# Kernel tuning notes

Hardware: AMD Instinct MI355X
Metric: run time of the kernel (lower is better)

Reference implementation:

```python
import jax, jax.numpy as jnp
import numpy as np

H = 16          # n_heads
D_MODEL = 1024
DK = D_MODEL // H  # 64
N = 2048        # total tokens (module flattens batch*seq)
NEG = -1000000000.0


def setup_inputs() -> dict:
    key = jax.random.key(0)
    ks = jax.random.split(key, 12)
    s = 1.0 / np.sqrt(D_MODEL)
    inp = {
        "query": jax.random.normal(ks[0], (N, D_MODEL), jnp.float32),
        "key": jax.random.normal(ks[1], (N, D_MODEL), jnp.float32),
        "value": jax.random.normal(ks[2], (N, D_MODEL), jnp.float32),
        "mask": jax.random.randint(ks[3], (1, N), 0, 2, jnp.int32),
        "Wq": jax.random.normal(ks[4], (D_MODEL, D_MODEL), jnp.float32) * s,
        "bq": jax.random.normal(ks[5], (D_MODEL,), jnp.float32) * 0.01,
        "Wk": jax.random.normal(ks[6], (D_MODEL, D_MODEL), jnp.float32) * s,
        "bk": jax.random.normal(ks[7], (D_MODEL,), jnp.float32) * 0.01,
        "Wv": jax.random.normal(ks[8], (D_MODEL, D_MODEL), jnp.float32) * s,
        "bv": jax.random.normal(ks[9], (D_MODEL,), jnp.float32) * 0.01,
        "Wo": jax.random.normal(ks[10], (D_MODEL, D_MODEL), jnp.float32) * s,
        "bo": jax.random.normal(ks[11], (D_MODEL,), jnp.float32) * 0.01,
    }
    return inp


def reference(query, key, value, mask, Wq, bq, Wk, bk, Wv, bv, Wo, bo):
    # Linear projections (torch Linear: x @ W.T + b), then split heads: (N, d_model) -> (h, N, d_k)
    def split_heads(x):
        return x.reshape(-1, H, DK).transpose(1, 0, 2)

    q = split_heads(query @ Wq.T + bq)
    k = split_heads(key @ Wk.T + bk)
    v = split_heads(value @ Wv.T + bv)

    # scaled dot-product attention: scores (h, N, N)
    scores = jnp.einsum("hnd,hmd->hnm", q, k) / jnp.sqrt(jnp.asarray(DK, q.dtype))
    # mask: (1, N) --unsqueeze(1)--> (1, 1, N), broadcast over (h, N, N)
    scores = jnp.where(mask[None, :, :] == 0, jnp.asarray(NEG, scores.dtype), scores)
    p_attn = jax.nn.softmax(scores, axis=-1)  # dropout identity (eval mode)

    x = jnp.einsum("hnm,hmd->hnd", p_attn, v)  # (h, N, d_k)
    x = x.transpose(1, 0, 2).reshape(-1, H * DK)  # (N, d_model)
    out = x @ Wo.T + bo
    return (out, p_attn)
```

## Files before the change

kernel.cpp:

```cpp
#include <hip/hip_runtime.h>


#define NTOK 2048
#define DMODEL 1024
#define NHEAD 16
#define DKH 64

typedef __attribute__((ext_vector_type(8))) short bf16x8;
typedef __attribute__((ext_vector_type(4))) float f32x4;

#define WAITVMC(n)                                          \
  do {                                                      \
    asm volatile("s_waitcnt vmcnt(" n ")" ::: "memory");    \
    __builtin_amdgcn_sched_barrier(0);                      \
  } while (0)
#define BARRIER()                                           \
  do {                                                      \
    __builtin_amdgcn_s_barrier();                           \
    __builtin_amdgcn_sched_barrier(0);                      \
  } while (0)

__device__ __forceinline__ unsigned short f2bf(float x) {
  unsigned int u = __builtin_bit_cast(unsigned int, x);
  u += 0x7fffu + ((u >> 16) & 1u);
  return (unsigned short)(u >> 16);
}

__device__ __forceinline__ void gl16(const void* g, void* l) {
  __builtin_amdgcn_global_load_lds((const __attribute__((address_space(1))) void*)g,
                                   (__attribute__((address_space(3))) void*)l, 16, 0, 0);
}

template<int ROWS>
__device__ __forceinline__ void stage_async(const unsigned short* src, int ld,
                                            char* lds, int w, int lane) {
  constexpr int RPW = ROWS / 4;
#pragma unroll
  for (int i = 0; i < RPW / 8; ++i) {
    const int row = w * RPW + i * 8 + (lane >> 3);
    const unsigned short* g = src + (size_t)row * ld + (((lane & 7) ^ (row & 7)) * 8);
    gl16(g, lds + (size_t)(w * RPW + i * 8) * 128);
  }
}

__device__ __forceinline__ bf16x8 ldsfrag(const char* lds, int r, int kb) {
  return *(const bf16x8*)(lds + r * 128 + (kb ^ ((r & 7) << 4)));
}

struct CvtP {
  const float* src[7];
  unsigned short* dst[7];
  int n8[8];
  const int* mask;
  float* mbias;
};
__global__ __launch_bounds__(256) void cvt_all(CvtP P) {
  const int a = blockIdx.z;
  const int i = blockIdx.x * 256 + threadIdx.x;
  if (i >= P.n8[a]) return;
  if (a == 7) {
#pragma unroll
    for (int r = 0; r < 8; ++r) {
      int j = i * 8 + r;
      P.mbias[j] = P.mask[j] ? 0.0f : -1e30f;
    }
    return;
  }
  const float4* s = (const float4*)P.src[a];
  float4 v0 = s[i * 2], v1 = s[i * 2 + 1];
  ushort4 h0, h1;
  h0.x = f2bf(v0.x); h0.y = f2bf(v0.y); h0.z = f2bf(v0.z); h0.w = f2bf(v0.w);
  h1.x = f2bf(v1.x); h1.y = f2bf(v1.y); h1.z = f2bf(v1.z); h1.w = f2bf(v1.w);
  ((ushort4*)P.dst[a])[i * 2] = h0;
  ((ushort4*)P.dst[a])[i * 2 + 1] = h1;
}

struct GemmP2 {
  const unsigned short* A[3];
  const unsigned short* B[3];
  const float* bias[3];
  unsigned short* Cb16;
  float* Cf32;
  unsigned short* VTd;
  long long sC;
  int lda, ldb, ldc, Nn, K;
};

template<int BM, bool OUTF32, bool VTRANS>
__global__ __launch_bounds__(256) void gemm_glds(GemmP2 P) {
  constexpr int BN = 128, WN = 64, FN = 4;
  constexpr int WM = BM / 2, FM = WM / 16;
  __shared__ char ldsA[BM * 128];
  __shared__ char ldsB[BN * 128];
  const int tid = threadIdx.x;
  const int lane = tid & 63, w = tid >> 6;
  const int l15 = lane & 15, lhi = lane >> 4;
  const int z = blockIdx.z;
  const int zi = (gridDim.z == 3) ? z : 0;
  const int ntn = P.Nn / BN;
  const int m0 = ((int)blockIdx.x / ntn) * BM;
  const int n0 = ((int)blockIdx.x % ntn) * BN;
  const unsigned short* Ab = P.A[zi] + (size_t)m0 * P.lda;
  const unsigned short* Bb = P.B[zi] + (size_t)n0 * P.ldb;
  const int wm = w >> 1, wn = w & 1;

  f32x4 acc[FM][FN] = {};
  for (int k0 = 0; k0 < P.K; k0 += 64) {
    stage_async<BM>(Ab + k0, P.lda, ldsA, w, lane);
    stage_async<BN>(Bb + k0, P.ldb, ldsB, w, lane);
    __syncthreads();
#pragma unroll
    for (int kk = 0; kk < 2; ++kk) {
      const int kb = kk * 64 + lhi * 16;
      bf16x8 a[FM], b[FN];
#pragma unroll
      for (int i = 0; i < FM; ++i) a[i] = ldsfrag(ldsA, wm * WM + i * 16 + l15, kb);
#pragma unroll
      for (int j = 0; j < FN; ++j) b[j] = ldsfrag(ldsB, wn * WN + j * 16 + l15, kb);
#pragma unroll
      for (int i = 0; i < FM; ++i)
#pragma unroll
        for (int j = 0; j < FN; ++j)
          acc[i][j] = __builtin_amdgcn_mfma_f32_16x16x32_bf16(a[i], b[j], acc[i][j], 0, 0, 0);
    }
    __syncthreads();
  }

  const int rbase = m0 + wm * WM + lhi * 4;
  const int cbase = n0 + wn * WN + l15;
  if (VTRANS && z == 2) {
#pragma unroll
    for (int j = 0; j < FN; ++j) {
      const int col = cbase + j * 16;
      const float badd = P.bias[zi][col];
#pragma unroll
      for (int i = 0; i < FM; ++i) {
        ushort4 t;
        t.x = f2bf(acc[i][j][0] + badd); t.y = f2bf(acc[i][j][1] + badd);
        t.z = f2bf(acc[i][j][2] + badd); t.w = f2bf(acc[i][j][3] + badd);
        *(ushort4*)(P.VTd + (size_t)col * NTOK + rbase + i * 16) = t;
      }
    }
    return;
  }
#pragma unroll
  for (int j = 0; j < FN; ++j) {
    const int col = cbase + j * 16;
    const float badd = P.bias[zi] ? P.bias[zi][col] : 0.0f;
#pragma unroll
    for (int i = 0; i < FM; ++i) {
#pragma unroll
      for (int rg = 0; rg < 4; ++rg) {
        const int row = rbase + i * 16 + rg;
        const float v = acc[i][j][rg] + badd;
        if constexpr (OUTF32)
          P.Cf32[(size_t)row * P.ldc + col] = v;
        else
          P.Cb16[(size_t)z * P.sC + (size_t)row * P.ldc + col] = f2bf(v);
      }
    }
  }
}

__global__ __launch_bounds__(512, 4) void attn7(const unsigned short* __restrict__ QP,
                                                const unsigned short* __restrict__ KP,
                                                const unsigned short* __restrict__ VT,
                                                const float* __restrict__ mbias,
                                                float* __restrict__ p,
                                                unsigned short* __restrict__ XB) {
  __shared__ char ldsK[2][2][64 * 128];
  __shared__ char ldsV[2][2][64 * 128];
  __shared__ char ldsP[2][64 * 128];
  const int tid = threadIdx.x;
  const int lane = tid & 63, w = tid >> 6;
  const int wm = w & 3, jg = w >> 2;
  const int l15 = lane & 15, lhi = lane >> 4;
  const int id = blockIdx.x;
  const int h = 2 * (id & 7) + ((id >> 3) & 1);
  const int q0 = (id >> 4) * 64;
  const int mrow = wm * 16 + l15;
  constexpr float CEXP = 0.1803368801111204f;

  {
    const int row = w * 8 + (lane >> 3);
    const unsigned short* g =
        QP + (size_t)(q0 + row) * DMODEL + h * DKH + (((lane & 7) ^ (row & 7)) * 8);
    gl16(g, ldsP[0] + (size_t)(w * 8) * 128);
  }
  __syncthreads();
  bf16x8 qf0 = ldsfrag(ldsP[0], mrow, lhi * 16);
  bf16x8 qf1 = ldsfrag(ldsP[0], mrow, 64 + lhi * 16);

  const unsigned short* Kh = KP + (size_t)(jg * 1024) * DMODEL + h * DKH;
  const unsigned short* Vh = VT + (size_t)h * DKH * NTOK + jg * 1024;
  const float* mbh = mbias + jg * 1024;

  float rsum = 0.0f;
  stage_async<64>(Kh, DMODEL, ldsK[jg][0], wm, lane);
  float4 m4n[4];
#pragma unroll
  for (int js = 0; js < 4; ++js) m4n[js] = *(const float4*)(mbh + js * 16 + lhi * 4);
  int b = 0;
  for (int it = 0; it < 16; ++it) {
    WAITVMC("0");
    BARRIER();
    if (it < 15)
      stage_async<64>(Kh + (size_t)(it + 1) * 64 * DMODEL, DMODEL, ldsK[jg][b ^ 1], wm, lane);
    float4 m4c[4];
#pragma unroll
    for (int js = 0; js < 4; ++js) m4c[js] = m4n[js];
    if (it < 15) {
      const float* mb = mbh + (it + 1) * 64;
#pragma unroll
      for (int js = 0; js < 4; ++js) m4n[js] = *(const float4*)(mb + js * 16 + lhi * 4);
    }
    __builtin_amdgcn_sched_barrier(0);
    f32x4 sacc[4] = {};
#pragma unroll
    for (int kk = 0; kk < 2; ++kk)
#pragma unroll
      for (int js = 0; js < 4; ++js) {
        bf16x8 kf = ldsfrag(ldsK[jg][b], js * 16 + l15, kk * 64 + lhi * 16);
        sacc[js] = __builtin_amdgcn_mfma_f32_16x16x32_bf16(kf, kk ? qf1 : qf0, sacc[js], 0, 0, 0);
      }
#pragma unroll
    for (int js = 0; js < 4; ++js) {
      rsum += exp2f(sacc[js][0] * CEXP + m4c[js].x);
      rsum += exp2f(sacc[js][1] * CEXP + m4c[js].y);
      rsum += exp2f(sacc[js][2] * CEXP + m4c[js].z);
      rsum += exp2f(sacc[js][3] * CEXP + m4c[js].w);
    }
    b ^= 1;
  }
  rsum += __shfl_xor(rsum, 16, 64);
  rsum += __shfl_xor(rsum, 32, 64);

  float* ldsR = (float*)ldsP[0];
  BARRIER();
  if (lane < 16) ldsR[jg * 64 + mrow] = rsum;
  BARRIER();
  const float rtot = ldsR[mrow] + ldsR[64 + mrow];
  const float lr = -log2f(rtot);

  f32x4 xacc[4] = {};
  stage_async<64>(Kh, DMODEL, ldsK[jg][0], wm, lane);
  stage_async<64>(Vh, NTOK, ldsV[jg][0], wm, lane);
#pragma unroll
  for (int js = 0; js < 4; ++js) m4n[js] = *(const float4*)(mbh + js * 16 + lhi * 4);
  b = 0;
  for (int it = 0; it < 16; ++it) {
    const int j0 = it * 64;
    if (it == 0) { WAITVMC("0"); } else { WAITVMC("4"); }
    BARRIER();
    if (it < 15) {
      stage_async<64>(Kh + (size_t)(j0 + 64) * DMODEL, DMODEL, ldsK[jg][b ^ 1], wm, lane);
      stage_async<64>(Vh + j0 + 64, NTOK, ldsV[jg][b ^ 1], wm, lane);
    }
    float4 m4c[4];
#pragma unroll
    for (int js = 0; js < 4; ++js) m4c[js] = m4n[js];
    if (it < 15) {
      const float* mb = mbh + (it + 1) * 64;
#pragma unroll
      for (int js = 0; js < 4; ++js) m4n[js] = *(const float4*)(mb + js * 16 + lhi * 4);
    }
    __builtin_amdgcn_sched_barrier(0);
    f32x4 sacc[4] = {};
#pragma unroll
    for (int kk = 0; kk < 2; ++kk)
#pragma unroll
      for (int js = 0; js < 4; ++js) {
        bf16x8 kf = ldsfrag(ldsK[jg][b], js * 16 + l15, kk * 64 + lhi * 16);
        sacc[js] = __builtin_amdgcn_mfma_f32_16x16x32_bf16(kf, kk ? qf1 : qf0, sacc[js], 0, 0, 0);
      }
#pragma unroll
    for (int js = 0; js < 4; ++js) {
      f32x4 e;
      e[0] = exp2f(sacc[js][0] * CEXP + (m4c[js].x + lr));
      e[1] = exp2f(sacc[js][1] * CEXP + (m4c[js].y + lr));
      e[2] = exp2f(sacc[js][2] * CEXP + (m4c[js].z + lr));
      e[3] = exp2f(sacc[js][3] * CEXP + (m4c[js].w + lr));
      ushort4 pb;
      pb.x = f2bf(e[0]); pb.y = f2bf(e[1]); pb.z = f2bf(e[2]); pb.w = f2bf(e[3]);
      *(ushort4*)(ldsP[jg] + mrow * 128 + ((js * 32 + lhi * 8) ^ ((mrow & 7) << 4))) = pb;
    }
#pragma unroll
    for (int jk = 0; jk < 2; ++jk) {
      bf16x8 pf = ldsfrag(ldsP[jg], mrow, jk * 64 + lhi * 16);
#pragma unroll
      for (int dd = 0; dd < 4; ++dd) {
        bf16x8 vf = ldsfrag(ldsV[jg][b], dd * 16 + l15, jk * 64 + lhi * 16);
        xacc[dd] = __builtin_amdgcn_mfma_f32_16x16x32_bf16(vf, pf, xacc[dd], 0, 0, 0);
      }
    }
#pragma unroll
    for (int r = 0; r < 4; ++r) {
      const int row = wm * 16 + r * 4 + lhi;
      const uint2 u =
          *(const uint2*)(ldsP[jg] + row * 128 + ((l15 * 8) ^ ((row & 7) << 4)));
      f32x4 f;
      f[0] = __builtin_bit_cast(float, u.x << 16);
      f[1] = __builtin_bit_cast(float, u.x & 0xffff0000u);
      f[2] = __builtin_bit_cast(float, u.y << 16);
      f[3] = __builtin_bit_cast(float, u.y & 0xffff0000u);
      __builtin_nontemporal_store(
          f, (f32x4*)(p + ((size_t)h * NTOK + q0 + row) * NTOK + jg * 1024 + j0 + l15 * 4));
    }
    b ^= 1;
  }

  float* ldsX = (float*)ldsK;
  BARRIER();
  if (jg == 1) {
#pragma unroll
    for (int dd = 0; dd < 4; ++dd) {
      const int off = (mrow * 256 + ((dd * 64 + lhi * 16) ^ ((mrow & 7) << 4))) >> 2;
      *(f32x4*)(ldsX + off) = xacc[dd];
    }
  }
  BARRIER();
  if (jg == 0) {
    unsigned short* xrow = XB + (size_t)(q0 + mrow) * DMODEL + h * DKH;
#pragma unroll
    for (int dd = 0; dd < 4; ++dd) {
      const int off = (mrow * 256 + ((dd * 64 + lhi * 16) ^ ((mrow & 7) << 4))) >> 2;
      f32x4 o = xacc[dd] + *(const f32x4*)(ldsX + off);
      ushort4 xb;
      xb.x = f2bf(o[0]); xb.y = f2bf(o[1]); xb.z = f2bf(o[2]); xb.w = f2bf(o[3]);
      *(ushort4*)(xrow + dd * 16 + lhi * 4) = xb;
    }
  }
}

extern "C" void kernel_launch(void* const* d_in, const int* in_sizes, int n_in,
                              void* d_out, int out_size, void* d_ws, size_t ws_size,
                              hipStream_t stream) {
  (void)in_sizes; (void)n_in; (void)out_size; (void)ws_size;
  const float* query = (const float*)d_in[0];
  const float* key_  = (const float*)d_in[1];
  const float* value = (const float*)d_in[2];
  const int*   mask  = (const int*)d_in[3];
  const float* Wq = (const float*)d_in[4];
  const float* bq = (const float*)d_in[5];
  const float* Wk = (const float*)d_in[6];
  const float* bk = (const float*)d_in[7];
  const float* Wv = (const float*)d_in[8];
  const float* bv = (const float*)d_in[9];
  const float* Wo = (const float*)d_in[10];
  const float* bo = (const float*)d_in[11];

  float* out = (float*)d_out;
  float* p = out + (size_t)NTOK * DMODEL;

  char* ws = (char*)d_ws;
  unsigned short* QP  = (unsigned short*)(ws);
  unsigned short* KP  = (unsigned short*)(ws + (4u << 20));
  unsigned short* VT  = (unsigned short*)(ws + (8u << 20));
  unsigned short* XB  = (unsigned short*)(ws + (12u << 20));
  unsigned short* qB  = (unsigned short*)(ws + (16u << 20));
  unsigned short* kB  = (unsigned short*)(ws + (20u << 20));
  unsigned short* vB  = (unsigned short*)(ws + (24u << 20));
  unsigned short* WqB = (unsigned short*)(ws + (28u << 20));
  unsigned short* WkB = (unsigned short*)(ws + (30u << 20));
  unsigned short* WvB = (unsigned short*)(ws + (32u << 20));
  unsigned short* WoB = (unsigned short*)(ws + (34u << 20));
  float* mbias = (float*)(ws + (36u << 20));

  {
    CvtP C = {};
    C.src[0] = query; C.dst[0] = qB;  C.n8[0] = NTOK * DMODEL / 8;
    C.src[1] = key_;  C.dst[1] = kB;  C.n8[1] = NTOK * DMODEL / 8;
    C.src[2] = value; C.dst[2] = vB;  C.n8[2] = NTOK * DMODEL / 8;
    C.src[3] = Wq;    C.dst[3] = WqB; C.n8[3] = DMODEL * DMODEL / 8;
    C.src[4] = Wk;    C.dst[4] = WkB; C.n8[4] = DMODEL * DMODEL / 8;
    C.src[5] = Wv;    C.dst[5] = WvB; C.n8[5] = DMODEL * DMODEL / 8;
    C.src[6] = Wo;    C.dst[6] = WoB; C.n8[6] = DMODEL * DMODEL / 8;
    C.n8[7] = NTOK / 8;
    C.mask = mask; C.mbias = mbias;
    cvt_all<<<dim3(1024, 1, 8), 256, 0, stream>>>(C);
  }
  {
    GemmP2 P = {};
    P.A[0] = qB; P.A[1] = kB; P.A[2] = vB;
    P.B[0] = WqB; P.B[1] = WkB; P.B[2] = WvB;
    P.bias[0] = bq; P.bias[1] = bk; P.bias[2] = bv;
    P.Cb16 = QP; P.VTd = VT; P.sC = (long long)NTOK * DMODEL;
    P.lda = DMODEL; P.ldb = DMODEL; P.ldc = DMODEL; P.Nn = DMODEL; P.K = DMODEL;
    gemm_glds<128, false, true>
        <<<dim3((NTOK / 128) * (DMODEL / 128), 1, 3), 256, 0, stream>>>(P);
  }
  attn7<<<dim3(512), 512, 0, stream>>>(QP, KP, VT, mbias, p, XB);
  {
    GemmP2 P = {};
    P.A[0] = XB; P.B[0] = WoB; P.bias[0] = bo;
    P.Cf32 = out; P.sC = 0;
    P.lda = DMODEL; P.ldb = DMODEL; P.ldc = DMODEL; P.Nn = DMODEL; P.K = DMODEL;
    gemm_glds<64, true, false>
        <<<dim3((NTOK / 64) * (DMODEL / 128), 1, 1), 256, 0, stream>>>(P);
  }
}
```

Measured before the change: 148.2 us.

## Rewrite attention kernel with 32x32x16 MFMA tiles and 4-wave blocks

```diff
diff --git a/kernel.cpp b/kernel.cpp
--- a/kernel.cpp
+++ b/kernel.cpp
@@ -8,6 +8,7 @@
 
 typedef __attribute__((ext_vector_type(8))) short bf16x8;
 typedef __attribute__((ext_vector_type(4))) float f32x4;
+typedef __attribute__((ext_vector_type(16))) float f32x16;
 
 #define WAITVMC(n)                                          \
   do {                                                      \
@@ -25,16 +26,19 @@
   u += 0x7fffu + ((u >> 16) & 1u);
   return (unsigned short)(u >> 16);
 }
+__device__ __forceinline__ unsigned int pkbf(float a, float b) {
+  return (unsigned int)f2bf(a) | ((unsigned int)f2bf(b) << 16);
+}
 
 __device__ __forceinline__ void gl16(const void* g, void* l) {
   __builtin_amdgcn_global_load_lds((const __attribute__((address_space(1))) void*)g,
                                    (__attribute__((address_space(3))) void*)l, 16, 0, 0);
 }
 
-template<int ROWS>
+template<int ROWS, int NW>
 __device__ __forceinline__ void stage_async(const unsigned short* src, int ld,
                                             char* lds, int w, int lane) {
-  constexpr int RPW = ROWS / 4;
+  constexpr int RPW = ROWS / NW;
 #pragma unroll
   for (int i = 0; i < RPW / 8; ++i) {
     const int row = w * RPW + i * 8 + (lane >> 3);
@@ -106,8 +110,8 @@
 
   f32x4 acc[FM][FN] = {};
   for (int k0 = 0; k0 < P.K; k0 += 64) {
-    stage_async<BM>(Ab + k0, P.lda, ldsA, w, lane);
-    stage_async<BN>(Bb + k0, P.ldb, ldsB, w, lane);
+    stage_async<BM, 4>(Ab + k0, P.lda, ldsA, w, lane);
+    stage_async<BN, 4>(Bb + k0, P.ldb, ldsB, w, lane);
     __syncthreads();
 #pragma unroll
     for (int kk = 0; kk < 2; ++kk) {
@@ -162,172 +166,185 @@
   }
 }
 
-__global__ __launch_bounds__(512, 4) void attn7(const unsigned short* __restrict__ QP,
+__global__ __launch_bounds__(256, 2) void attn8(const unsigned short* __restrict__ QP,
                                                 const unsigned short* __restrict__ KP,
                                                 const unsigned short* __restrict__ VT,
                                                 const float* __restrict__ mbias,
                                                 float* __restrict__ p,
                                                 unsigned short* __restrict__ XB) {
-  __shared__ char ldsK[2][2][64 * 128];
-  __shared__ char ldsV[2][2][64 * 128];
-  __shared__ char ldsP[2][64 * 128];
+  __shared__ char LDS[81920];
   const int tid = threadIdx.x;
   const int lane = tid & 63, w = tid >> 6;
-  const int wm = w & 3, jg = w >> 2;
-  const int l15 = lane & 15, lhi = lane >> 4;
+  const int rg = w >> 1, jg = w & 1;
+  const int m31 = lane & 31, hi = lane >> 5;
   const int id = blockIdx.x;
   const int h = 2 * (id & 7) + ((id >> 3) & 1);
   const int q0 = (id >> 4) * 64;
-  const int mrow = wm * 16 + l15;
+  const int row_q = rg * 32 + m31;
+  const int swq = (row_q & 7) << 4;
+  const int swm = (m31 & 7) << 4;
   constexpr float CEXP = 0.1803368801111204f;
 
-  {
-    const int row = w * 8 + (lane >> 3);
-    const unsigned short* g =
-        QP + (size_t)(q0 + row) * DMODEL + h * DKH + (((lane & 7) ^ (row & 7)) * 8);
-    gl16(g, ldsP[0] + (size_t)(w * 8) * 128);
-  }
+  char* ldsKb[2] = {LDS + jg * 16384, LDS + jg * 16384 + 8192};
+  char* ldsVb[2] = {LDS + 32768 + jg * 16384, LDS + 32768 + jg * 16384 + 8192};
+  char* ldsPj = LDS + 65536 + jg * 8192;
+  char* ldsQ = LDS + 65536;
+  float* ldsR = (float*)(LDS + 65536 + 8192);
+
+  stage_async<64, 4>(QP + (size_t)q0 * DMODEL + h * DKH, DMODEL, ldsQ, w, lane);
   __syncthreads();
-  bf16x8 qf0 = ldsfrag(ldsP[0], mrow, lhi * 16);
-  bf16x8 qf1 = ldsfrag(ldsP[0], mrow, 64 + lhi * 16);
+  bf16x8 qf[4];
+#pragma unroll
+  for (int kt = 0; kt < 4; ++kt)
+    qf[kt] = *(const bf16x8*)(ldsQ + row_q * 128 + ((kt * 32 + hi * 16) ^ swq));
 
   const unsigned short* Kh = KP + (size_t)(jg * 1024) * DMODEL + h * DKH;
   const unsigned short* Vh = VT + (size_t)h * DKH * NTOK + jg * 1024;
   const float* mbh = mbias + jg * 1024;
 
   float rsum = 0.0f;
-  stage_async<64>(Kh, DMODEL, ldsK[jg][0], wm, lane);
-  float4 m4n[4];
-#pragma unroll
-  for (int js = 0; js < 4; ++js) m4n[js] = *(const float4*)(mbh + js * 16 + lhi * 4);
+  float4 m4[8];
+  stage_async<64, 2>(Kh, DMODEL, ldsKb[0], rg, lane);
+#pragma unroll
+  for (int q = 0; q < 8; ++q)
+    m4[q] = *(const float4*)(mbh + (q >> 2) * 32 + (q & 3) * 8 + hi * 4);
   int b = 0;
   for (int it = 0; it < 16; ++it) {
-    WAITVMC("0");
+    WAITVMC("8");
     BARRIER();
     if (it < 15)
-      stage_async<64>(Kh + (size_t)(it + 1) * 64 * DMODEL, DMODEL, ldsK[jg][b ^ 1], wm, lane);
-    float4 m4c[4];
-#pragma unroll
-    for (int js = 0; js < 4; ++js) m4c[js] = m4n[js];
+      stage_async<64, 2>(Kh + (size_t)(it + 1) * 64 * DMODEL, DMODEL, ldsKb[b ^ 1], rg, lane);
+    __builtin_amdgcn_sched_barrier(0);
+    f32x16 s0 = {}, s1 = {};
+#pragma unroll
+    for (int kt = 0; kt < 4; ++kt) {
+      bf16x8 k0 = *(const bf16x8*)(ldsKb[b] + m31 * 128 + ((kt * 32 + hi * 16) ^ swm));
+      bf16x8 k1 = *(const bf16x8*)(ldsKb[b] + (32 + m31) * 128 + ((kt * 32 + hi * 16) ^ swm));
+      s0 = __builtin_amdgcn_mfma_f32_32x32x16_bf16(k0, qf[kt], s0, 0, 0, 0);
+      s1 = __builtin_amdgcn_mfma_f32_32x32x16_bf16(k1, qf[kt], s1, 0, 0, 0);
+    }
+#pragma unroll
+    for (int rq = 0; rq < 4; ++rq) {
+      rsum += exp2f(s0[rq * 4 + 0] * CEXP + m4[rq].x) + exp2f(s0[rq * 4 + 1] * CEXP + m4[rq].y) +
+              exp2f(s0[rq * 4 + 2] * CEXP + m4[rq].z) + exp2f(s0[rq * 4 + 3] * CEXP + m4[rq].w);
+      rsum += exp2f(s1[rq * 4 + 0] * CEXP + m4[4 + rq].x) + exp2f(s1[rq * 4 + 1] * CEXP + m4[4 + rq].y) +
+              exp2f(s1[rq * 4 + 2] * CEXP + m4[4 + rq].z) + exp2f(s1[rq * 4 + 3] * CEXP + m4[4 + rq].w);
+    }
     if (it < 15) {
-      const float* mb = mbh + (it + 1) * 64;
-#pragma unroll
-      for (int js = 0; js < 4; ++js) m4n[js] = *(const float4*)(mb + js * 16 + lhi * 4);
-    }
-    __builtin_amdgcn_sched_barrier(0);
-    f32x4 sacc[4] = {};
-#pragma unroll
-    for (int kk = 0; kk < 2; ++kk)
-#pragma unroll
-      for (int js = 0; js < 4; ++js) {
-        bf16x8 kf = ldsfrag(ldsK[jg][b], js * 16 + l15, kk * 64 + lhi * 16);
-        sacc[js] = __builtin_amdgcn_mfma_f32_16x16x32_bf16(kf, kk ? qf1 : qf0, sacc[js], 0, 0, 0);
-      }
-#pragma unroll
-    for (int js = 0; js < 4; ++js) {
-      rsum += exp2f(sacc[js][0] * CEXP + m4c[js].x);
-      rsum += exp2f(sacc[js][1] * CEXP + m4c[js].y);
-      rsum += exp2f(sacc[js][2] * CEXP + m4c[js].z);
-      rsum += exp2f(sacc[js][3] * CEXP + m4c[js].w);
+      const float* mb2 = mbh + (it + 1) * 64;
+#pragma unroll
+      for (int q = 0; q < 8; ++q)
+        m4[q] = *(const float4*)(mb2 + (q >> 2) * 32 + (q & 3) * 8 + hi * 4);
     }
     b ^= 1;
   }
-  rsum += __shfl_xor(rsum, 16, 64);
   rsum += __shfl_xor(rsum, 32, 64);
-
-  float* ldsR = (float*)ldsP[0];
+  if (lane < 32) ldsR[jg * 64 + row_q] = rsum;
   BARRIER();
-  if (lane < 16) ldsR[jg * 64 + mrow] = rsum;
-  BARRIER();
-  const float rtot = ldsR[mrow] + ldsR[64 + mrow];
-  const float lr = -log2f(rtot);
-
-  f32x4 xacc[4] = {};
-  stage_async<64>(Kh, DMODEL, ldsK[jg][0], wm, lane);
-  stage_async<64>(Vh, NTOK, ldsV[jg][0], wm, lane);
-#pragma unroll
-  for (int js = 0; js < 4; ++js) m4n[js] = *(const float4*)(mbh + js * 16 + lhi * 4);
+  const float lr = -log2f(ldsR[row_q] + ldsR[64 + row_q]);
+
+  f32x16 x0 = {}, x1 = {};
+  stage_async<64, 2>(Kh, DMODEL, ldsKb[0], rg, lane);
+  stage_async<64, 2>(Vh, NTOK, ldsVb[0], rg, lane);
+#pragma unroll
+  for (int q = 0; q < 8; ++q)
+    m4[q] = *(const float4*)(mbh + (q >> 2) * 32 + (q & 3) * 8 + hi * 4);
   b = 0;
   for (int it = 0; it < 16; ++it) {
     const int j0 = it * 64;
-    if (it == 0) { WAITVMC("0"); } else { WAITVMC("4"); }
+    if (it == 0) { WAITVMC("8"); } else { WAITVMC("16"); }
     BARRIER();
     if (it < 15) {
-      stage_async<64>(Kh + (size_t)(j0 + 64) * DMODEL, DMODEL, ldsK[jg][b ^ 1], wm, lane);
-      stage_async<64>(Vh + j0 + 64, NTOK, ldsV[jg][b ^ 1], wm, lane);
-    }
-    float4 m4c[4];
-#pragma unroll
-    for (int js = 0; js < 4; ++js) m4c[js] = m4n[js];
+      stage_async<64, 2>(Kh + (size_t)(j0 + 64) * DMODEL, DMODEL, ldsKb[b ^ 1], rg, lane);
+      stage_async<64, 2>(Vh + j0 + 64, NTOK, ldsVb[b ^ 1], rg, lane);
+    }
+    __builtin_amdgcn_sched_barrier(0);
+    f32x16 s0 = {}, s1 = {};
+#pragma unroll
+    for (int kt = 0; kt < 4; ++kt) {
+      bf16x8 k0 = *(const bf16x8*)(ldsKb[b] + m31 * 128 + ((kt * 32 + hi * 16) ^ swm));
+      bf16x8 k1 = *(const bf16x8*)(ldsKb[b] + (32 + m31) * 128 + ((kt * 32 + hi * 16) ^ swm));
+      s0 = __builtin_amdgcn_mfma_f32_32x32x16_bf16(k0, qf[kt], s0, 0, 0, 0);
+      s1 = __builtin_amdgcn_mfma_f32_32x32x16_bf16(k1, qf[kt], s1, 0, 0, 0);
+    }
+#pragma unroll
+    for (int rq = 0; rq < 4; ++rq) {
+      uint2 u;
+      u.x = pkbf(exp2f(s0[rq * 4 + 0] * CEXP + m4[rq].x + lr),
+                 exp2f(s0[rq * 4 + 1] * CEXP + m4[rq].y + lr));
+      u.y = pkbf(exp2f(s0[rq * 4 + 2] * CEXP + m4[rq].z + lr),
+                 exp2f(s0[rq * 4 + 3] * CEXP + m4[rq].w + lr));
+      *(uint2*)(ldsPj + row_q * 128 + ((rq * 16 + hi * 8) ^ swq)) = u;
+      uint2 v;
+      v.x = pkbf(exp2f(s1[rq * 4 + 0] * CEXP + m4[4 + rq].x + lr),
+                 exp2f(s1[rq * 4 + 1] * CEXP + m4[4 + rq].y + lr));
+      v.y = pkbf(exp2f(s1[rq * 4 + 2] * CEXP + m4[4 + rq].z + lr),
+                 exp2f(s1[rq * 4 + 3] * CEXP + m4[4 + rq].w + lr));
+      *(uint2*)(ldsPj + row_q * 128 + ((64 + rq * 16 + hi * 8) ^ swq)) = v;
+    }
+#pragma unroll
+    for (int ks = 0; ks < 4; ++ks) {
+      bf16x8 pf = *(const bf16x8*)(ldsPj + row_q * 128 + ((ks * 32 + hi * 16) ^ swq));
+      bf16x8 v0 = *(const bf16x8*)(ldsVb[b] + m31 * 128 + ((ks * 32 + hi * 16) ^ swm));
+      bf16x8 v1 = *(const bf16x8*)(ldsVb[b] + (32 + m31) * 128 + ((ks * 32 + hi * 16) ^ swm));
+      x0 = __builtin_amdgcn_mfma_f32_32x32x16_bf16(v0, pf, x0, 0, 0, 0);
+      x1 = __builtin_amdgcn_mfma_f32_32x32x16_bf16(v1, pf, x1, 0, 0, 0);
+    }
     if (it < 15) {
-      const float* mb = mbh + (it + 1) * 64;
-#pragma unroll
-      for (int js = 0; js < 4; ++js) m4n[js] = *(const float4*)(mb + js * 16 + lhi * 4);
-    }
-    __builtin_amdgcn_sched_barrier(0);
-    f32x4 sacc[4] = {};
-#pragma unroll
-    for (int kk = 0; kk < 2; ++kk)
-#pragma unroll
-      for (int js = 0; js < 4; ++js) {
-        bf16x8 kf = ldsfrag(ldsK[jg][b], js * 16 + l15, kk * 64 + lhi * 16);
-        sacc[js] = __builtin_amdgcn_mfma_f32_16x16x32_bf16(kf, kk ? qf1 : qf0, sacc[js], 0, 0, 0);
+      const float* mb2 = mbh + (j0 + 64);
+#pragma unroll
+      for (int q = 0; q < 8; ++q)
+        m4[q] = *(const float4*)(mb2 + (q >> 2) * 32 + (q & 3) * 8 + hi * 4);
+    }
+    float* pb = p + ((size_t)h * NTOK + q0) * NTOK + jg * 1024 + j0;
+#pragma unroll
+    for (int rb = 0; rb < 4; ++rb) {
+      const int rr = rg * 32 + rb * 8 + (lane >> 3);
+      const int swr = (rr & 7) << 4;
+#pragma unroll
+      for (int hh = 0; hh < 2; ++hh) {
+        const uint2 u = *(const uint2*)(ldsPj + rr * 128 + ((((lane & 7) * 8) + hh * 64) ^ swr));
+        f32x4 f;
+        f[0] = __builtin_bit_cast(float, u.x << 16);
+        f[1] = __builtin_bit_cast(float, u.x & 0xffff0000u);
+        f[2] = __builtin_bit_cast(float, u.y << 16);
+        f[3] = __builtin_bit_cast(float, u.y & 0xffff0000u);
+        __builtin_nontemporal_store(f, (f32x4*)(pb + (size_t)rr * NTOK + hh * 32 + (lane & 7) * 4));
       }
-#pragma unroll
-    for (int js = 0; js < 4; ++js) {
-      f32x4 e;
-      e[0] = exp2f(sacc[js][0] * CEXP + (m4c[js].x + lr));
-      e[1] = exp2f(sacc[js][1] * CEXP + (m4c[js].y + lr));
-      e[2] = exp2f(sacc[js][2] * CEXP + (m4c[js].z + lr));
-      e[3] = exp2f(sacc[js][3] * CEXP + (m4c[js].w + lr));
-      ushort4 pb;
-      pb.x = f2bf(e[0]); pb.y = f2bf(e[1]); pb.z = f2bf(e[2]); pb.w = f2bf(e[3]);
-      *(ushort4*)(ldsP[jg] + mrow * 128 + ((js * 32 + lhi * 8) ^ ((mrow & 7) << 4))) = pb;
-    }
-#pragma unroll
-    for (int jk = 0; jk < 2; ++jk) {
-      bf16x8 pf = ldsfrag(ldsP[jg], mrow, jk * 64 + lhi * 16);
-#pragma unroll
-      for (int dd = 0; dd < 4; ++dd) {
-        bf16x8 vf = ldsfrag(ldsV[jg][b], dd * 16 + l15, jk * 64 + lhi * 16);
-        xacc[dd] = __builtin_amdgcn_mfma_f32_16x16x32_bf16(vf, pf, xacc[dd], 0, 0, 0);
-      }
-    }
-#pragma unroll
-    for (int r = 0; r < 4; ++r) {
-      const int row = wm * 16 + r * 4 + lhi;
-      const uint2 u =
-          *(const uint2*)(ldsP[jg] + row * 128 + ((l15 * 8) ^ ((row & 7) << 4)));
-      f32x4 f;
-      f[0] = __builtin_bit_cast(float, u.x << 16);
-      f[1] = __builtin_bit_cast(float, u.x & 0xffff0000u);
-      f[2] = __builtin_bit_cast(float, u.y << 16);
-      f[3] = __builtin_bit_cast(float, u.y & 0xffff0000u);
-      __builtin_nontemporal_store(
-          f, (f32x4*)(p + ((size_t)h * NTOK + q0 + row) * NTOK + jg * 1024 + j0 + l15 * 4));
     }
     b ^= 1;
   }
 
-  float* ldsX = (float*)ldsK;
+  float* ldsX = (float*)LDS;
   BARRIER();
   if (jg == 1) {
 #pragma unroll
-    for (int dd = 0; dd < 4; ++dd) {
-      const int off = (mrow * 256 + ((dd * 64 + lhi * 16) ^ ((mrow & 7) << 4))) >> 2;
-      *(f32x4*)(ldsX + off) = xacc[dd];
+    for (int db = 0; db < 2; ++db) {
+      const f32x16 xx = db ? x1 : x0;
+#pragma unroll
+      for (int rq = 0; rq < 4; ++rq) {
+        f32x4 v;
+        v[0] = xx[rq * 4 + 0]; v[1] = xx[rq * 4 + 1];
+        v[2] = xx[rq * 4 + 2]; v[3] = xx[rq * 4 + 3];
+        *(f32x4*)((char*)ldsX + row_q * 256 + ((db * 128 + rq * 32 + hi * 16) ^ swq)) = v;
+      }
     }
   }
   BARRIER();
   if (jg == 0) {
-    unsigned short* xrow = XB + (size_t)(q0 + mrow) * DMODEL + h * DKH;
-#pragma unroll
-    for (int dd = 0; dd < 4; ++dd) {
-      const int off = (mrow * 256 + ((dd * 64 + lhi * 16) ^ ((mrow & 7) << 4))) >> 2;
-      f32x4 o = xacc[dd] + *(const f32x4*)(ldsX + off);
-      ushort4 xb;
-      xb.x = f2bf(o[0]); xb.y = f2bf(o[1]); xb.z = f2bf(o[2]); xb.w = f2bf(o[3]);
-      *(ushort4*)(xrow + dd * 16 + lhi * 4) = xb;
+    unsigned short* xr = XB + (size_t)(q0 + row_q) * DMODEL + h * DKH;
+#pragma unroll
+    for (int db = 0; db < 2; ++db) {
+      const f32x16 xx = db ? x1 : x0;
+#pragma unroll
+      for (int rq = 0; rq < 4; ++rq) {
+        f32x4 o = *(const f32x4*)((char*)ldsX + row_q * 256 + ((db * 128 + rq * 32 + hi * 16) ^ swq));
+        o[0] += xx[rq * 4 + 0]; o[1] += xx[rq * 4 + 1];
+        o[2] += xx[rq * 4 + 2]; o[3] += xx[rq * 4 + 3];
+        ushort4 t;
+        t.x = f2bf(o[0]); t.y = f2bf(o[1]); t.z = f2bf(o[2]); t.w = f2bf(o[3]);
+        *(ushort4*)(xr + db * 32 + rq * 8 + hi * 4) = t;
+      }
     }
   }
 }
@@ -389,7 +406,7 @@
     gemm_glds<128, false, true>
         <<<dim3((NTOK / 128) * (DMODEL / 128), 1, 3), 256, 0, stream>>>(P);
   }
-  attn7<<<dim3(512), 512, 0, stream>>>(QP, KP, VT, mbias, p, XB);
+  attn8<<<dim3(512), 256, 0, stream>>>(QP, KP, VT, mbias, p, XB);
   {
     GemmP2 P = {};
     P.A[0] = XB; P.B[0] = WoB; P.bias[0] = bo;
```

Result: no change. 148.7 us (+0.4%).
